# Kernel optimization log

Measured on AMD Instinct MI355X. Metric: run time of the kernel, lower is better.

Reference implementation:

```python
import jax, jax.numpy as jnp
import numpy as np

HEADS = 4
DIM_HEAD = 32
SCALE = DIM_HEAD ** -0.5
GN_EPS = 1e-5


def setup_inputs() -> dict:
    key = jax.random.key(0)
    k1, k2, k3 = jax.random.split(key, 3)
    dim, hidden = 64, HEADS * DIM_HEAD
    x = jax.random.normal(k1, (2, dim, 32, 32, 32), dtype=jnp.float32)
    w_qkv = jax.random.normal(k2, (3 * hidden, dim), dtype=jnp.float32) * (dim ** -0.5)
    w_out = jax.random.normal(k3, (dim, hidden), dtype=jnp.float32) * (hidden ** -0.5)
    b_out = jnp.zeros((dim,), dtype=jnp.float32)
    gn_w = jnp.ones((dim,), dtype=jnp.float32)
    gn_b = jnp.zeros((dim,), dtype=jnp.float32)
    return {"x": x, "w_qkv": w_qkv, "w_out": w_out, "b_out": b_out, "gn_w": gn_w, "gn_b": gn_b}


def reference(x, w_qkv, w_out, b_out, gn_w, gn_b):
    b, c, D, H, W = x.shape
    n = D * H * W
    xf = x.reshape(b, c, n)  # flatten spatial: 1x1 Conv3d == channel matmul
    qkv = jnp.einsum('oc,bcn->bon', w_qkv, xf)  # [b, 3*hidden, n]
    q, k, v = jnp.split(qkv, 3, axis=1)
    rs = lambda t: t.reshape(b, HEADS, DIM_HEAD, n)  # b h d n
    q, k, v = rs(q), rs(k), rs(v)
    q = jax.nn.softmax(q, axis=2) * SCALE   # softmax over head-dim channels
    k = jax.nn.softmax(k, axis=3)           # softmax over spatial positions
    context = jnp.einsum('bhdn,bhen->bhde', k, v)   # [b, h, d, e], tiny
    out = jnp.einsum('bhde,bhdn->bhen', context, q)  # [b, h, e, n]
    out = out.reshape(b, HEADS * DIM_HEAD, n)
    # to_out: 1x1 Conv3d with bias, then GroupNorm(1, dim)
    y = jnp.einsum('oc,bcn->bon', w_out, out) + b_out[None, :, None]
    mean = jnp.mean(y, axis=(1, 2), keepdims=True)
    var = jnp.var(y, axis=(1, 2), keepdims=True)
    y = (y - mean) * jax.lax.rsqrt(var + GN_EPS)
    y = y * gn_w[None, :, None] + gn_b[None, :, None]
    return y.reshape(b, -1, D, H, W)
```

## Files before the change

### kernel.cpp

```cpp
#include <hip/hip_runtime.h>
#include <hip/hip_bf16.h>

#define NB 2
#define C_IN 64
#define N_SP 32768
#define NHEADS 4
#define DH 32
#define HID 128
#define QK_SCALE 0.17677669529663687f
#define GN_EPS_C 1e-5f
#define NGN 2097152.0f

using bf16x8 = __attribute__((ext_vector_type(8))) short;
using f32x4  = __attribute__((ext_vector_type(4))) float;
using u16x4  = __attribute__((ext_vector_type(4))) unsigned short;
using u16x8  = __attribute__((ext_vector_type(8))) unsigned short;

__device__ __forceinline__ unsigned short f2bf(float f) {
    union { float f; unsigned u; } c{f};
    unsigned r = c.u + 0x7FFFu + ((c.u >> 16) & 1u);
    return (unsigned short)(r >> 16);
}
__device__ __forceinline__ float bf2f(unsigned short u) {
    union { unsigned u; float f; } c{ (unsigned)u << 16 };
    return c.f;
}

__device__ __forceinline__ void load_xf(const float* __restrict__ xb, int n0,
        int lg, int lc, bf16x8 xf[2][2]) {
#pragma unroll
    for (int s = 0; s < 2; ++s) {
        int n = n0 + s * 16 + lc;
#pragma unroll
        for (int kk = 0; kk < 2; ++kk) {
            bf16x8 v;
#pragma unroll
            for (int j = 0; j < 8; ++j)
                v[j] = (short)f2bf(xb[(size_t)(kk * 32 + lg * 8 + j) * N_SP + n]);
            xf[s][kk] = v;
        }
    }
}

__global__ __launch_bounds__(512) void kA(const float* __restrict__ x,
        const float* __restrict__ wqkv, unsigned short* __restrict__ qs_frag,
        float* __restrict__ ctx_part, float* __restrict__ ksum_part) {
    __shared__ unsigned short wl[3072 * 8];
    __shared__ unsigned short kt[2][8192];
    __shared__ unsigned short vt[2][8192];
    const int t = threadIdx.x, wv = t >> 6, l = t & 63, lg = l >> 4, lc = l & 15;
    const int blk = blockIdx.x;
    const int b = blk >> 7, nblk = blk & 127;
    const int n0 = nblk * 256 + wv * 32;

    bf16x8 xf[2][2];
    load_xf(x + (size_t)b * C_IN * N_SP, n0, lg, lc, xf);

#pragma unroll
    for (int i = 0; i < 6; ++i) {
        int idx = t + i * 512;
        int f = idx >> 6, lane = idx & 63;
        int row = (f >> 1) * 16 + (lane & 15);
        int c0 = (f & 1) * 32 + (lane >> 4) * 8;
        const float* wp = wqkv + row * 64 + c0;
        u16x8 pk;
#pragma unroll
        for (int j = 0; j < 8; ++j) pk[j] = f2bf(wp[j]);
        *(u16x8*)(wl + (size_t)idx * 8) = pk;
    }
    __syncthreads();

#pragma unroll
    for (int h = 0; h < NHEADS; ++h) {
        f32x4 qa[2][2] = {};
#pragma unroll
        for (int mi = 0; mi < 2; ++mi)
#pragma unroll
            for (int kk = 0; kk < 2; ++kk) {
                bf16x8 aq = *(const bf16x8*)(wl + ((size_t)((h * 2 + mi) * 2 + kk) * 64 + l) * 8);
#pragma unroll
                for (int s = 0; s < 2; ++s)
                    qa[mi][s] = __builtin_amdgcn_mfma_f32_16x16x32_bf16(aq, xf[s][kk], qa[mi][s], 0, 0, 0);
            }
#pragma unroll
        for (int s = 0; s < 2; ++s) {
            float sum = 0.f;
#pragma unroll
            for (int mi = 0; mi < 2; ++mi)
#pragma unroll
                for (int r = 0; r < 4; ++r) {
                    float e = __expf(qa[mi][s][r]);
                    qa[mi][s][r] = e; sum += e;
                }
            sum += __shfl_xor(sum, 16);
            sum += __shfl_xor(sum, 32);
            float inv = QK_SCALE / sum;
            int pos16 = nblk * 16 + wv * 2 + s;
            unsigned short* blob = qs_frag + ((size_t)(b * 2048 + pos16) * 4 + h) * 512;
#pragma unroll
            for (int mi = 0; mi < 2; ++mi) {
                u16x4 pk;
#pragma unroll
                for (int r = 0; r < 4; ++r) pk[r] = f2bf(qa[mi][s][r] * inv);
                int lanep = (mi * 2 + (lg >> 1)) * 16 + lc;
                *(u16x4*)(blob + (size_t)lanep * 8 + (lg & 1) * 4) = pk;
            }
        }
    }

    const int di = (wv >> 1) & 1, ei = wv & 1;
#pragma unroll
    for (int h = 0; h < NHEADS; ++h) {
        const int bs = h & 1;
        f32x4 ka[2][2] = {}, va[2][2] = {};
#pragma unroll
        for (int e = 0; e < 2; ++e)
#pragma unroll
            for (int kk = 0; kk < 2; ++kk) {
                bf16x8 wk = *(const bf16x8*)(wl + ((size_t)((8 + 2 * h + e) * 2 + kk) * 64 + l) * 8);
                bf16x8 wf = *(const bf16x8*)(wl + ((size_t)((16 + 2 * h + e) * 2 + kk) * 64 + l) * 8);
#pragma unroll
                for (int s = 0; s < 2; ++s) {
                    ka[s][e] = __builtin_amdgcn_mfma_f32_16x16x32_bf16(xf[s][kk], wk, ka[s][e], 0, 0, 0);
                    va[s][e] = __builtin_amdgcn_mfma_f32_16x16x32_bf16(xf[s][kk], wf, va[s][e], 0, 0, 0);
                }
            }
#pragma unroll
        for (int s = 0; s < 2; ++s)
#pragma unroll
            for (int e = 0; e < 2; ++e) {
                u16x4 pk, pv;
#pragma unroll
                for (int r = 0; r < 4; ++r) {
                    pk[r] = f2bf(__expf(ka[s][e][r]));
                    pv[r] = f2bf(va[s][e][r]);
                }
                int ch = e * 16 + lc;
                int pos = wv * 32 + s * 16 + lg * 4;
                int ba = (ch * 512 + pos * 2) ^ ((ch & 7) << 4);
                *(u16x4*)((char*)kt[bs] + ba) = pk;
                *(u16x4*)((char*)vt[bs] + ba) = pv;
            }
        __syncthreads();
        if (wv < 4) {
            f32x4 ca = {};
            float ks = 0.f;
#pragma unroll
            for (int k0 = 0; k0 < 256; k0 += 32) {
                int ar = di * 16 + lc, br = ei * 16 + lc;
                bf16x8 af = *(const bf16x8*)((const char*)kt[bs] + ((ar * 512 + (k0 + lg * 8) * 2) ^ ((ar & 7) << 4)));
                bf16x8 bf = *(const bf16x8*)((const char*)vt[bs] + ((br * 512 + (k0 + lg * 8) * 2) ^ ((br & 7) << 4)));
                if (ei == 0) {
#pragma unroll
                    for (int j = 0; j < 8; ++j) ks += bf2f((unsigned short)af[j]);
                }
                ca = __builtin_amdgcn_mfma_f32_16x16x32_bf16(af, bf, ca, 0, 0, 0);
            }
            float* cp = ctx_part + ((size_t)(b * 4 + h) * 128 + nblk) * 1024;
#pragma unroll
            for (int r = 0; r < 4; ++r)
                cp[(di * 16 + lg * 4 + r) * 32 + ei * 16 + lc] = ca[r];
            if (ei == 0) {
                ks += __shfl_xor(ks, 16);
                ks += __shfl_xor(ks, 32);
                if (lg == 0)
                    ksum_part[((size_t)(b * 4 + h) * 128 + nblk) * 32 + di * 16 + lc] = ks;
            }
        }
    }
}

__global__ __launch_bounds__(256) void kB(const float* __restrict__ ctx_part,
        const float* __restrict__ ksum_part, const float* __restrict__ wout,
        unsigned short* __restrict__ weff) {
    __shared__ float c8[8][32];
    __shared__ float cred[32];
    __shared__ float ksr[2];
    __shared__ float ksv;
    const int blk = blockIdx.x;
    const int g = blk >> 5, ds = blk & 31;
    const int bb = g >> 2, h = g & 3;
    const int t = threadIdx.x;
    const int e = t & 31, ii = t >> 5;
    float a = 0.f;
    const float* cp = ctx_part + (size_t)g * 128 * 1024 + ds * 32 + e;
#pragma unroll 4
    for (int i = ii * 16; i < ii * 16 + 16; ++i) a += cp[(size_t)i * 1024];
    c8[ii][e] = a;
    float ks = 0.f;
    if (t < 128) ks = ksum_part[((size_t)g * 128 + t) * 32 + ds];
#pragma unroll
    for (int off = 32; off > 0; off >>= 1) ks += __shfl_down(ks, off, 64);
    if (t < 128 && (t & 63) == 0) ksr[t >> 6] = ks;
    __syncthreads();
    if (t < 32) {
        float s = 0.f;
#pragma unroll
        for (int k = 0; k < 8; ++k) s += c8[k][t];
        cred[t] = s;
    }
    if (t == 0) ksv = ksr[0] + ksr[1];
    __syncthreads();
    if (t < 64) {
        const float* wrow = wout + t * HID + h * 32;
        float acc = 0.f;
#pragma unroll
        for (int e2 = 0; e2 < 32; ++e2) acc = fmaf(wrow[e2], cred[e2], acc);
        acc /= ksv;
        weff[((size_t)bb * 64 + t) * 128 + h * 32 + ds] = f2bf(acc);
    }
}

__global__ __launch_bounds__(256) void kC(const unsigned short* __restrict__ qs_frag,
        const unsigned short* __restrict__ weff, const float* __restrict__ bout,
        unsigned short* __restrict__ y_t, float* __restrict__ pstats) {
    __shared__ float red[8];
    const int t = threadIdx.x, wv = t >> 6, l = t & 63, lg = l >> 4, lc = l & 15;
    const int blk = blockIdx.x;
    const int b = blk >> 8, nblk = blk & 255;
    const int n0 = nblk * 128 + wv * 32;

    f32x4 acc[4][2] = {};
    const unsigned short* wb = weff + (size_t)b * 8192;
#pragma unroll
    for (int kk = 0; kk < 4; ++kk) {
        bf16x8 bq[2];
#pragma unroll
        for (int s = 0; s < 2; ++s) {
            int pos16 = nblk * 8 + wv * 2 + s;
            bq[s] = *(const bf16x8*)(qs_frag +
                ((size_t)(b * 2048 + pos16) * 4 + kk) * 512 + (size_t)l * 8);
        }
#pragma unroll
        for (int mt = 0; mt < 4; ++mt) {
            bf16x8 af = *(const bf16x8*)(wb + (size_t)(mt * 16 + lc) * 128 + kk * 32 + lg * 8);
#pragma unroll
            for (int s = 0; s < 2; ++s)
                acc[mt][s] = __builtin_amdgcn_mfma_f32_16x16x32_bf16(af, bq[s], acc[mt][s], 0, 0, 0);
        }
    }
    float s1 = 0.f, s2 = 0.f;
#pragma unroll
    for (int mt = 0; mt < 4; ++mt) {
        float bo[4];
#pragma unroll
        for (int r = 0; r < 4; ++r) bo[r] = bout[mt * 16 + lg * 4 + r];
#pragma unroll
        for (int s = 0; s < 2; ++s) {
            u16x4 pk;
#pragma unroll
            for (int r = 0; r < 4; ++r) {
                float val = acc[mt][s][r] + bo[r];
                s1 += val;
                s2 = fmaf(val, val, s2);
                pk[r] = f2bf(val);
            }
            int n = n0 + s * 16 + lc;
            *(u16x4*)(y_t + ((size_t)b * N_SP + n) * 64 + mt * 16 + lg * 4) = pk;
        }
    }
#pragma unroll
    for (int off = 32; off > 0; off >>= 1) {
        s1 += __shfl_down(s1, off, 64);
        s2 += __shfl_down(s2, off, 64);
    }
    if (l == 0) { red[wv * 2] = s1; red[wv * 2 + 1] = s2; }
    __syncthreads();
    if (t == 0) {
        float S1 = red[0] + red[2] + red[4] + red[6];
        float S2 = red[1] + red[3] + red[5] + red[7];
        pstats[(b * 256 + nblk) * 2]     = S1;
        pstats[(b * 256 + nblk) * 2 + 1] = S2;
    }
}

__global__ __launch_bounds__(256) void kE(const unsigned short* __restrict__ y_t,
        const float* __restrict__ pstats, const float* __restrict__ gnw,
        const float* __restrict__ gnb, float* __restrict__ out) {
    __shared__ float red[8];
    __shared__ float ms[2];
    __shared__ float w2s[64], b2s[64];
    const int t = threadIdx.x;
    const int blk = blockIdx.x;
    const int b = blk >> 9, nb = blk & 511;
    float s1 = pstats[(b * 256 + t) * 2];
    float s2 = pstats[(b * 256 + t) * 2 + 1];
#pragma unroll
    for (int off = 32; off > 0; off >>= 1) {
        s1 += __shfl_down(s1, off, 64);
        s2 += __shfl_down(s2, off, 64);
    }
    if ((t & 63) == 0) { red[(t >> 6) * 2] = s1; red[(t >> 6) * 2 + 1] = s2; }
    __syncthreads();
    if (t == 0) {
        float S1 = red[0] + red[2] + red[4] + red[6];
        float S2 = red[1] + red[3] + red[5] + red[7];
        float mean = S1 / NGN;
        float var = S2 / NGN - mean * mean;
        ms[0] = mean; ms[1] = rsqrtf(var + GN_EPS_C);
    }
    __syncthreads();
    if (t < 64) {
        float w2 = gnw[t] * ms[1];
        w2s[t] = w2;
        b2s[t] = gnb[t] - ms[0] * w2;
    }
    __syncthreads();
    const int n = nb * 64 + (t & 63), o0 = (t >> 6) * 16;
    const unsigned short* yp = y_t + ((size_t)b * N_SP + n) * 64 + o0;
    u16x8 v0 = *(const u16x8*)yp;
    u16x8 v1 = *(const u16x8*)(yp + 8);
    float* ob = out + (size_t)b * C_IN * N_SP + n;
#pragma unroll
    for (int j = 0; j < 8; ++j)
        ob[(size_t)(o0 + j) * N_SP] = fmaf(bf2f((unsigned short)v0[j]), w2s[o0 + j], b2s[o0 + j]);
#pragma unroll
    for (int j = 0; j < 8; ++j)
        ob[(size_t)(o0 + 8 + j) * N_SP] = fmaf(bf2f((unsigned short)v1[j]), w2s[o0 + 8 + j], b2s[o0 + 8 + j]);
}

extern "C" void kernel_launch(void* const* d_in, const int* in_sizes, int n_in,
                              void* d_out, int out_size, void* d_ws, size_t ws_size,
                              hipStream_t stream) {
    const float* x    = (const float*)d_in[0];
    const float* wqkv = (const float*)d_in[1];
    const float* wout = (const float*)d_in[2];
    const float* bout = (const float*)d_in[3];
    const float* gnw  = (const float*)d_in[4];
    const float* gnb  = (const float*)d_in[5];
    float* out = (float*)d_out;

    char* ws = (char*)d_ws;
    size_t off = 0;
    unsigned short* qs_frag = (unsigned short*)(ws + off); off += (size_t)NB * 2048 * 4 * 512 * 2;
    float* ctx_part  = (float*)(ws + off); off += (size_t)8 * 128 * 1024 * 4;
    float* ksum_part = (float*)(ws + off); off += (size_t)8 * 128 * 32 * 4;
    unsigned short* weff = (unsigned short*)(ws + off); off += 2 * 8192 * 2;
    unsigned short* y_t  = (unsigned short*)(ws + off); off += (size_t)NB * N_SP * 64 * 2;
    float* pstats = (float*)(ws + off); off += NB * 256 * 2 * 4;

    kA<<<dim3(256), dim3(512), 0, stream>>>(x, wqkv, qs_frag, ctx_part, ksum_part);
    kB<<<dim3(256), dim3(256), 0, stream>>>(ctx_part, ksum_part, wout, weff);
    kC<<<dim3(512), dim3(256), 0, stream>>>(qs_frag, weff, bout, y_t, pstats);
    kE<<<dim3(1024), dim3(256), 0, stream>>>(y_t, pstats, gnw, gnb, out);
}
```

Measured before the change: 41.24 us.

## Recompute output projection in GroupNorm kernel instead of storing bf16 intermediate

The stats kernel no longer writes the bf16 projected output to workspace; it only computes per-block sums. The final kernel recomputes the MFMA projection from the q fragments and effective weights, applies the fused bias and GroupNorm affine, and transposes through shared memory for coalesced fp32 stores. This removes an 8 MB write and read of the intermediate at the cost of doing the small projection GEMM twice and using about 33 KB of LDS per block. The output is also no longer rounded to bf16 before normalisation.

```diff
diff --git a/kernel.cpp b/kernel.cpp
--- a/kernel.cpp
+++ b/kernel.cpp
@@ -213,12 +213,11 @@
 
 __global__ __launch_bounds__(256) void kC(const unsigned short* __restrict__ qs_frag,
         const unsigned short* __restrict__ weff, const float* __restrict__ bout,
-        unsigned short* __restrict__ y_t, float* __restrict__ pstats) {
+        float* __restrict__ pstats) {
     __shared__ float red[8];
     const int t = threadIdx.x, wv = t >> 6, l = t & 63, lg = l >> 4, lc = l & 15;
     const int blk = blockIdx.x;
     const int b = blk >> 8, nblk = blk & 255;
-    const int n0 = nblk * 128 + wv * 32;
 
     f32x4 acc[4][2] = {};
     const unsigned short* wb = weff + (size_t)b * 8192;
@@ -246,18 +245,13 @@
 #pragma unroll
         for (int r = 0; r < 4; ++r) bo[r] = bout[mt * 16 + lg * 4 + r];
 #pragma unroll
-        for (int s = 0; s < 2; ++s) {
-            u16x4 pk;
+        for (int s = 0; s < 2; ++s)
 #pragma unroll
             for (int r = 0; r < 4; ++r) {
                 float val = acc[mt][s][r] + bo[r];
                 s1 += val;
                 s2 = fmaf(val, val, s2);
-                pk[r] = f2bf(val);
-            }
-            int n = n0 + s * 16 + lc;
-            *(u16x4*)(y_t + ((size_t)b * N_SP + n) * 64 + mt * 16 + lg * 4) = pk;
-        }
+            }
     }
 #pragma unroll
     for (int off = 32; off > 0; off >>= 1) {
@@ -274,15 +268,18 @@
     }
 }
 
-__global__ __launch_bounds__(256) void kE(const unsigned short* __restrict__ y_t,
+__global__ __launch_bounds__(256) void kE(const unsigned short* __restrict__ qs_frag,
+        const unsigned short* __restrict__ weff, const float* __restrict__ bout,
         const float* __restrict__ pstats, const float* __restrict__ gnw,
         const float* __restrict__ gnb, float* __restrict__ out) {
     __shared__ float red[8];
     __shared__ float ms[2];
     __shared__ float w2s[64], b2s[64];
-    const int t = threadIdx.x;
+    __shared__ float yl[128 * 65];
+    const int t = threadIdx.x, wv = t >> 6, l = t & 63, lg = l >> 4, lc = l & 15;
     const int blk = blockIdx.x;
-    const int b = blk >> 9, nb = blk & 511;
+    const int b = blk >> 8, nblk = blk & 255;
+
     float s1 = pstats[(b * 256 + t) * 2];
     float s2 = pstats[(b * 256 + t) * 2 + 1];
 #pragma unroll
@@ -290,7 +287,7 @@
         s1 += __shfl_down(s1, off, 64);
         s2 += __shfl_down(s2, off, 64);
     }
-    if ((t & 63) == 0) { red[(t >> 6) * 2] = s1; red[(t >> 6) * 2 + 1] = s2; }
+    if (l == 0) { red[wv * 2] = s1; red[wv * 2 + 1] = s2; }
     __syncthreads();
     if (t == 0) {
         float S1 = red[0] + red[2] + red[4] + red[6];
@@ -303,20 +300,47 @@
     if (t < 64) {
         float w2 = gnw[t] * ms[1];
         w2s[t] = w2;
-        b2s[t] = gnb[t] - ms[0] * w2;
-    }
-    __syncthreads();
-    const int n = nb * 64 + (t & 63), o0 = (t >> 6) * 16;
-    const unsigned short* yp = y_t + ((size_t)b * N_SP + n) * 64 + o0;
-    u16x8 v0 = *(const u16x8*)yp;
-    u16x8 v1 = *(const u16x8*)(yp + 8);
+        b2s[t] = (bout[t] - ms[0]) * w2 + gnb[t];
+    }
+
+    f32x4 acc[4][2] = {};
+    const unsigned short* wb = weff + (size_t)b * 8192;
+#pragma unroll
+    for (int kk = 0; kk < 4; ++kk) {
+        bf16x8 bq[2];
+#pragma unroll
+        for (int s = 0; s < 2; ++s) {
+            int pos16 = nblk * 8 + wv * 2 + s;
+            bq[s] = *(const bf16x8*)(qs_frag +
+                ((size_t)(b * 2048 + pos16) * 4 + kk) * 512 + (size_t)l * 8);
+        }
+#pragma unroll
+        for (int mt = 0; mt < 4; ++mt) {
+            bf16x8 af = *(const bf16x8*)(wb + (size_t)(mt * 16 + lc) * 128 + kk * 32 + lg * 8);
+#pragma unroll
+            for (int s = 0; s < 2; ++s)
+                acc[mt][s] = __builtin_amdgcn_mfma_f32_16x16x32_bf16(af, bq[s], acc[mt][s], 0, 0, 0);
+        }
+    }
+    __syncthreads();
+#pragma unroll
+    for (int mt = 0; mt < 4; ++mt)
+#pragma unroll
+        for (int s = 0; s < 2; ++s)
+#pragma unroll
+            for (int r = 0; r < 4; ++r) {
+                int o = mt * 16 + lg * 4 + r;
+                int pos = wv * 32 + s * 16 + lc;
+                yl[pos * 65 + o] = fmaf(acc[mt][s][r], w2s[o], b2s[o]);
+            }
+    __syncthreads();
+    const int p = t & 127, oh = (t >> 7) * 32;
+    const int n = nblk * 128 + p;
     float* ob = out + (size_t)b * C_IN * N_SP + n;
-#pragma unroll
-    for (int j = 0; j < 8; ++j)
-        ob[(size_t)(o0 + j) * N_SP] = fmaf(bf2f((unsigned short)v0[j]), w2s[o0 + j], b2s[o0 + j]);
-#pragma unroll
-    for (int j = 0; j < 8; ++j)
-        ob[(size_t)(o0 + 8 + j) * N_SP] = fmaf(bf2f((unsigned short)v1[j]), w2s[o0 + 8 + j], b2s[o0 + 8 + j]);
+    const float* yr = yl + p * 65 + oh;
+#pragma unroll
+    for (int j = 0; j < 32; ++j)
+        ob[(size_t)(oh + j) * N_SP] = yr[j];
 }
 
 extern "C" void kernel_launch(void* const* d_in, const int* in_sizes, int n_in,
@@ -336,11 +360,10 @@
     float* ctx_part  = (float*)(ws + off); off += (size_t)8 * 128 * 1024 * 4;
     float* ksum_part = (float*)(ws + off); off += (size_t)8 * 128 * 32 * 4;
     unsigned short* weff = (unsigned short*)(ws + off); off += 2 * 8192 * 2;
-    unsigned short* y_t  = (unsigned short*)(ws + off); off += (size_t)NB * N_SP * 64 * 2;
     float* pstats = (float*)(ws + off); off += NB * 256 * 2 * 4;
 
     kA<<<dim3(256), dim3(512), 0, stream>>>(x, wqkv, qs_frag, ctx_part, ksum_part);
     kB<<<dim3(256), dim3(256), 0, stream>>>(ctx_part, ksum_part, wout, weff);
-    kC<<<dim3(512), dim3(256), 0, stream>>>(qs_frag, weff, bout, y_t, pstats);
-    kE<<<dim3(1024), dim3(256), 0, stream>>>(y_t, pstats, gnw, gnb, out);
-}
+    kC<<<dim3(512), dim3(256), 0, stream>>>(qs_frag, weff, bout, pstats);
+    kE<<<dim3(512), dim3(256), 0, stream>>>(qs_frag, weff, bout, pstats, gnw, gnb, out);
+}
```

New measurement: 43.80 us. +6.2%, slower.

## Shrink kA shared memory to raise occupancy, reload K/V weights after Q phase

Applied to the files above, without the earlier changes.

Kernel kA drops its double-buffered K/V tiles for single buffers. It also stages only the Q weights at first, then reloads the K and V weight slices into the same LDS region after the Q phase, which cuts LDS from about 112KB to 64KB. A launch-bounds hint asks for 4 waves per SIMD. This should let two 512-thread blocks sit on one CU. The cost is extra __syncthreads, a second weight conversion pass, and the loss of overlap between heads now that the buffer is single.

```diff
diff --git a/kernel.cpp b/kernel.cpp
--- a/kernel.cpp
+++ b/kernel.cpp
@@ -42,12 +42,12 @@
     }
 }
 
-__global__ __launch_bounds__(512) void kA(const float* __restrict__ x,
+__global__ __launch_bounds__(512, 4) void kA(const float* __restrict__ x,
         const float* __restrict__ wqkv, unsigned short* __restrict__ qs_frag,
         float* __restrict__ ctx_part, float* __restrict__ ksum_part) {
-    __shared__ unsigned short wl[3072 * 8];
-    __shared__ unsigned short kt[2][8192];
-    __shared__ unsigned short vt[2][8192];
+    __shared__ unsigned short wl[2048 * 8];
+    __shared__ unsigned short kt[8192];
+    __shared__ unsigned short vt[8192];
     const int t = threadIdx.x, wv = t >> 6, l = t & 63, lg = l >> 4, lc = l & 15;
     const int blk = blockIdx.x;
     const int b = blk >> 7, nblk = blk & 127;
@@ -57,7 +57,7 @@
     load_xf(x + (size_t)b * C_IN * N_SP, n0, lg, lc, xf);
 
 #pragma unroll
-    for (int i = 0; i < 6; ++i) {
+    for (int i = 0; i < 2; ++i) {
         int idx = t + i * 512;
         int f = idx >> 6, lane = idx & 63;
         int row = (f >> 1) * 16 + (lane & 15);
@@ -107,24 +107,39 @@
             }
         }
     }
+    __syncthreads();
+
+#pragma unroll
+    for (int i = 0; i < 4; ++i) {
+        int idx = t + i * 512;
+        int f = idx >> 6, lane = idx & 63;
+        int row = (8 + (f >> 1)) * 16 + (lane & 15);
+        int c0 = (f & 1) * 32 + (lane >> 4) * 8;
+        const float* wp = wqkv + row * 64 + c0;
+        u16x8 pk;
+#pragma unroll
+        for (int j = 0; j < 8; ++j) pk[j] = f2bf(wp[j]);
+        *(u16x8*)(wl + (size_t)idx * 8) = pk;
+    }
+    __syncthreads();
 
     const int di = (wv >> 1) & 1, ei = wv & 1;
 #pragma unroll
     for (int h = 0; h < NHEADS; ++h) {
-        const int bs = h & 1;
         f32x4 ka[2][2] = {}, va[2][2] = {};
 #pragma unroll
         for (int e = 0; e < 2; ++e)
 #pragma unroll
             for (int kk = 0; kk < 2; ++kk) {
-                bf16x8 wk = *(const bf16x8*)(wl + ((size_t)((8 + 2 * h + e) * 2 + kk) * 64 + l) * 8);
-                bf16x8 wf = *(const bf16x8*)(wl + ((size_t)((16 + 2 * h + e) * 2 + kk) * 64 + l) * 8);
+                bf16x8 wk = *(const bf16x8*)(wl + ((size_t)((2 * h + e) * 2 + kk) * 64 + l) * 8);
+                bf16x8 wf = *(const bf16x8*)(wl + ((size_t)(16 + (2 * h + e) * 2 + kk) * 64 + l) * 8);
 #pragma unroll
                 for (int s = 0; s < 2; ++s) {
                     ka[s][e] = __builtin_amdgcn_mfma_f32_16x16x32_bf16(xf[s][kk], wk, ka[s][e], 0, 0, 0);
                     va[s][e] = __builtin_amdgcn_mfma_f32_16x16x32_bf16(xf[s][kk], wf, va[s][e], 0, 0, 0);
                 }
             }
+        __syncthreads();
 #pragma unroll
         for (int s = 0; s < 2; ++s)
 #pragma unroll
@@ -138,8 +153,8 @@
                 int ch = e * 16 + lc;
                 int pos = wv * 32 + s * 16 + lg * 4;
                 int ba = (ch * 512 + pos * 2) ^ ((ch & 7) << 4);
-                *(u16x4*)((char*)kt[bs] + ba) = pk;
-                *(u16x4*)((char*)vt[bs] + ba) = pv;
+                *(u16x4*)((char*)kt + ba) = pk;
+                *(u16x4*)((char*)vt + ba) = pv;
             }
         __syncthreads();
         if (wv < 4) {
@@ -148,8 +163,8 @@
 #pragma unroll
             for (int k0 = 0; k0 < 256; k0 += 32) {
                 int ar = di * 16 + lc, br = ei * 16 + lc;
-                bf16x8 af = *(const bf16x8*)((const char*)kt[bs] + ((ar * 512 + (k0 + lg * 8) * 2) ^ ((ar & 7) << 4)));
-                bf16x8 bf = *(const bf16x8*)((const char*)vt[bs] + ((br * 512 + (k0 + lg * 8) * 2) ^ ((br & 7) << 4)));
+                bf16x8 af = *(const bf16x8*)((const char*)kt + ((ar * 512 + (k0 + lg * 8) * 2) ^ ((ar & 7) << 4)));
+                bf16x8 bf = *(const bf16x8*)((const char*)vt + ((br * 512 + (k0 + lg * 8) * 2) ^ ((br & 7) << 4)));
                 if (ei == 0) {
 #pragma unroll
                     for (int j = 0; j < 8; ++j) ks += bf2f((unsigned short)af[j]);
```

After: 42.38 us. 2.8% more time.
